# Optimization experiments

Measured on AMD Instinct MI355X. Metric: run time of the kernel, lower is better.

Reference implementation:

```python
import jax, jax.numpy as jnp
import numpy as np

B, S, D, H, F, V, K = 8, 1024, 1024, 16, 4096, 8192, 64
HD = D // H
ALPHA = 0.1


def layernorm(x, g, b, eps=1e-5):
    mu = jnp.mean(x, axis=-1, keepdims=True)
    var = jnp.var(x, axis=-1, keepdims=True)
    return (x - mu) * jax.lax.rsqrt(var + eps) * g + b


def setup_inputs() -> dict:
    key = jax.random.key(0)
    ks = jax.random.split(key, 16)
    s = lambda fan: 1.0 / np.sqrt(fan)
    inp = {
        "x": jax.random.normal(ks[0], (B, S, D), jnp.float32),
        "token_ids": jax.random.randint(ks[1], (B, S), 0, V),
        "pmi": jax.random.normal(ks[2], (V, V), jnp.float32) * 0.1,
        "Wq": jax.random.normal(ks[3], (D, D), jnp.float32) * s(D),
        "bq": jnp.zeros((D,), jnp.float32),
        "Wk": jax.random.normal(ks[4], (D, D), jnp.float32) * s(D),
        "bk": jnp.zeros((D,), jnp.float32),
        "Wv": jax.random.normal(ks[5], (D, D), jnp.float32) * s(D),
        "bv": jnp.zeros((D,), jnp.float32),
        "Wo": jax.random.normal(ks[6], (D, D), jnp.float32) * s(D),
        "bo": jnp.zeros((D,), jnp.float32),
        "W1": jax.random.normal(ks[7], (D, F), jnp.float32) * s(D),
        "b1": jnp.zeros((F,), jnp.float32),
        "W2": jax.random.normal(ks[8], (F, D), jnp.float32) * s(F),
        "b2": jnp.zeros((D,), jnp.float32),
        "g1": jnp.ones((D,), jnp.float32),
        "be1": jnp.zeros((D,), jnp.float32),
        "g2": jnp.ones((D,), jnp.float32),
        "be2": jnp.zeros((D,), jnp.float32),
    }
    return inp


def reference(x, token_ids, pmi, Wq, bq, Wk, bk, Wv, bv, Wo, bo,
              W1, b1, W2, b2, g1, be1, g2, be2):
    # --- SparseStatAttention: QK^T + alpha*PMI bias, top-k mask, softmax ---
    q = (x @ Wq + bq).reshape(B, S, H, HD)
    k = (x @ Wk + bk).reshape(B, S, H, HD)
    v = (x @ Wv + bv).reshape(B, S, H, HD)
    scores = jnp.einsum("bihd,bjhd->bhij", q, k) / np.sqrt(HD)  # [B,H,S,S]
    bias = pmi[token_ids[:, :, None], token_ids[:, None, :]]     # [B,S,S]
    scores = scores + ALPHA * bias[:, None, :, :]
    # top-k sparsification per query row (threshold at k-th largest value)
    kth = jax.lax.top_k(scores, K)[0][..., -1:]
    scores = jnp.where(scores >= kth, scores, -jnp.inf)
    w = jax.nn.softmax(scores, axis=-1)
    attn = jnp.einsum("bhij,bjhd->bihd", w, v).reshape(B, S, D)
    attn = attn @ Wo + bo
    # --- residual + norm1 (dropout is identity in eval) ---
    h = layernorm(x + attn, g1, be1)
    # --- GELU FFN (torch nn.GELU default = exact erf) ---
    ff = jax.nn.gelu(h @ W1 + b1, approximate=False) @ W2 + b2
    return layernorm(h + ff, g2, be2)
```

## Files before the change

### kernel.cpp

```cpp
#include <hip/hip_runtime.h>
#include <cstdint>
#include <cstddef>

#define B_   8
#define S_   1024
#define D_   1024
#define H_   16
#define HD_  64
#define F_   4096
#define V_   8192
#define KTOP 64

typedef unsigned short ushort_t;
typedef __attribute__((ext_vector_type(8))) short short8;
typedef __attribute__((ext_vector_type(8))) _Float16 half8;
typedef __attribute__((ext_vector_type(4))) float floatx4;
typedef __attribute__((ext_vector_type(4))) unsigned int uintx4;
typedef __attribute__((ext_vector_type(4))) float floatv4;
typedef __attribute__((ext_vector_type(4))) unsigned short ushortx4;
typedef __attribute__((ext_vector_type(8))) unsigned short ushortx8;

__device__ __forceinline__ ushort_t f2bf(float f) {
    unsigned int u = __builtin_bit_cast(unsigned int, f);
    u += 0x7fffu + ((u >> 16) & 1u);
    return (ushort_t)(u >> 16);
}
__device__ __forceinline__ float bf2f(ushort_t u) {
    unsigned int x = ((unsigned int)u) << 16;
    return __builtin_bit_cast(float, x);
}
__device__ __forceinline__ ushort_t f2h(float f) {
    _Float16 h = (_Float16)f;
    return __builtin_bit_cast(ushort_t, h);
}
__device__ __forceinline__ float h2f(ushort_t u) {
    return (float)__builtin_bit_cast(_Float16, u);
}

__device__ __forceinline__ void gload_lds16(const ushort_t* g, ushort_t* lds_base) {
    __builtin_amdgcn_global_load_lds(
        (const __attribute__((address_space(1))) unsigned int*)g,
        (__attribute__((address_space(3))) unsigned int*)lds_base,
        16, 0, 0);
}

__global__ __launch_bounds__(256) void cast_x_kernel(const float* __restrict__ x,
                                                     ushort_t* __restrict__ xb) {
    int gid = blockIdx.x * 256 + threadIdx.x;
    floatv4 v = ((const floatv4*)x)[gid];
    ushortx4 o;
    o[0] = f2bf(v[0]); o[1] = f2bf(v[1]); o[2] = f2bf(v[2]); o[3] = f2bf(v[3]);
    ((ushortx4*)xb)[gid] = o;
}

__global__ void transpose_cast_kernel(const float* __restrict__ W, ushort_t* __restrict__ WT,
                                      int K, int N, float scale) {
    __shared__ float tile[32][33];
    int n0 = blockIdx.x * 32, k0 = blockIdx.y * 32;
    #pragma unroll
    for (int i = threadIdx.y; i < 32; i += 8)
        tile[i][threadIdx.x] = W[(size_t)(k0 + i) * N + n0 + threadIdx.x];
    __syncthreads();
    #pragma unroll
    for (int i = threadIdx.y; i < 32; i += 8)
        WT[(size_t)(n0 + i) * K + k0 + threadIdx.x] = f2bf(tile[threadIdx.x][i] * scale);
}

__global__ __launch_bounds__(256) void pack_bias3_kernel(const float* __restrict__ bq,
                                                         const float* __restrict__ bk,
                                                         const float* __restrict__ bv,
                                                         float* __restrict__ o) {
    int i = blockIdx.x * 256 + threadIdx.x;
    float v = (i < 1024) ? bq[i] * 0.125f : (i < 2048) ? bk[i - 1024] : bv[i - 2048];
    o[i] = v;
}

__global__ __launch_bounds__(256) void bias_gather_kernel(const int* __restrict__ tok,
                                                          const float* __restrict__ pmi,
                                                          ushort_t* __restrict__ biasb) {
    int b = blockIdx.x >> 10;
    int i = blockIdx.x & (S_ - 1);
    int ti = tok[b * S_ + i];
    const float* prow = pmi + (size_t)ti * V_;
    #pragma unroll
    for (int it = 0; it < 4; it++) {
        int j = threadIdx.x + it * 256;
        int tj = tok[b * S_ + j];
        biasb[(size_t)blockIdx.x * S_ + j] = f2h(0.1f * prow[tj]);
    }
}

__global__ __launch_bounds__(256) void transpose_v_kernel(const ushort_t* __restrict__ v,
                                                          ushort_t* __restrict__ vT) {
    __shared__ ushort_t t[64 * 72];
    int bh = blockIdx.x >> 4;
    int s0 = (blockIdx.x & 15) * 64;
    #pragma unroll
    for (int it = 0; it < 2; it++) {
        int idx = threadIdx.x + it * 256;
        int sl = idx >> 3, dg = (idx & 7) * 8;
        *(uintx4*)&t[sl * 72 + dg] = *(const uintx4*)&v[((size_t)bh * S_ + s0 + sl) * HD_ + dg];
    }
    __syncthreads();
    #pragma unroll
    for (int it = 0; it < 2; it++) {
        int idx = threadIdx.x + it * 256;
        int dl = idx >> 3, sg = (idx & 7) * 8;
        ushortx8 o;
        #pragma unroll
        for (int i = 0; i < 8; i++) o[i] = f2h(bf2f(t[(sg + i) * 72 + dl]));
        *(ushortx8*)&vT[((size_t)bh * HD_ + dl) * S_ + s0 + sg] = o;
    }
}

__global__ __launch_bounds__(256) void gemm_bt(const ushort_t* __restrict__ A,
                                               const ushort_t* __restrict__ BT,
                                               const float* __restrict__ bias,
                                               ushort_t* __restrict__ C,
                                               int M, int N, int K, int ep) {
    __shared__ ushort_t As[2][128 * 32];
    __shared__ ushort_t Bs[2][128 * 32];

    const int tid = threadIdx.x;
    const int wid = tid >> 6, lane = tid & 63;
    const int quad = lane >> 4, r = lane & 15;
    const int wr = wid >> 1, wc = wid & 1;
    const int m0 = blockIdx.y * 128, n0 = blockIdx.x * 128;

    floatx4 acc[4][4];
    #pragma unroll
    for (int a = 0; a < 4; a++)
        #pragma unroll
        for (int b = 0; b < 4; b++) acc[a][b] = (floatx4){0.f, 0.f, 0.f, 0.f};

    const int srow = wid * 16 + (lane >> 2);
    const int scol = (lane & 3) * 8;
    const ushort_t* Ag0 = A + (size_t)(m0 + srow) * K + scol;
    const ushort_t* Ag1 = A + (size_t)(m0 + 64 + srow) * K + scol;
    const ushort_t* Bg0 = BT + (size_t)(n0 + srow) * K + scol;
    const ushort_t* Bg1 = BT + (size_t)(n0 + 64 + srow) * K + scol;
    const int d0 = (wid * 16) * 32;
    const int d1 = (64 + wid * 16) * 32;

    gload_lds16(Ag0, &As[0][d0]);
    gload_lds16(Ag1, &As[0][d1]);
    gload_lds16(Bg0, &Bs[0][d0]);
    gload_lds16(Bg1, &Bs[0][d1]);
    __syncthreads();

    int cur = 0;
    for (int k0 = 0; k0 < K; k0 += 32) {
        const int nxt = cur ^ 1;
        if (k0 + 32 < K) {
            gload_lds16(Ag0 + k0 + 32, &As[nxt][d0]);
            gload_lds16(Ag1 + k0 + 32, &As[nxt][d1]);
            gload_lds16(Bg0 + k0 + 32, &Bs[nxt][d0]);
            gload_lds16(Bg1 + k0 + 32, &Bs[nxt][d1]);
        }
        short8 af[4], bf[4];
        #pragma unroll
        for (int t = 0; t < 4; t++)
            af[t] = *(const short8*)&As[cur][(wr * 64 + t * 16 + r) * 32 + quad * 8];
        #pragma unroll
        for (int t = 0; t < 4; t++)
            bf[t] = *(const short8*)&Bs[cur][(wc * 64 + t * 16 + r) * 32 + quad * 8];
        #pragma unroll
        for (int tm = 0; tm < 4; tm++)
            #pragma unroll
            for (int tn = 0; tn < 4; tn++)
                acc[tm][tn] = __builtin_amdgcn_mfma_f32_16x16x32_bf16(af[tm], bf[tn], acc[tm][tn], 0, 0, 0);
        __syncthreads();
        cur = nxt;
    }

    #pragma unroll
    for (int tm = 0; tm < 4; tm++) {
        #pragma unroll
        for (int tn = 0; tn < 4; tn++) {
            const int n = n0 + wc * 64 + tn * 16 + r;
            const float bv = bias[n];
            #pragma unroll
            for (int i2 = 0; i2 < 4; i2++) {
                const int m = m0 + wr * 64 + tm * 16 + quad * 4 + i2;
                float v = acc[tm][tn][i2] + bv;
                if (ep == 1) v = 0.5f * v * (1.0f + erff(v * 0.70710678118654752f));
                size_t idx;
                if (ep == 2) {
                    int tensor = n >> 10, nn = n & 1023;
                    idx = (size_t)tensor * (B_ * S_ * D_)
                        + (((size_t)(m >> 10) * H_ + (nn >> 6)) * S_ + (m & (S_ - 1))) * HD_ + (nn & (HD_ - 1));
                } else {
                    idx = (size_t)m * N + n;
                }
                C[idx] = f2bf(v);
            }
        }
    }
}

__global__ __launch_bounds__(256) void attn_kernel(const ushort_t* __restrict__ q,
                                                   const ushort_t* __restrict__ k,
                                                   const ushort_t* __restrict__ vT,
                                                   const ushort_t* __restrict__ biasb,
                                                   ushort_t* __restrict__ attnb) {
    extern __shared__ char smem[];
    ushort_t* Sm = (ushort_t*)smem;
    _Float16* Smh = (_Float16*)smem;

    const int bid = blockIdx.x;
    const int b = bid >> 10;
    const int h = (bid >> 6) & (H_ - 1);
    const int i0 = (bid & 63) * 16;
    const int tid = threadIdx.x;
    const int wid = tid >> 6, lane = tid & 63;
    const int quad = lane >> 4, r = lane & 15;

    const size_t bh = (size_t)b * H_ + h;
    const ushort_t* qbase = q + bh * S_ * HD_;
    const ushort_t* kbase = k + bh * S_ * HD_;
    const ushort_t* vbase = vT + bh * HD_ * S_;
    const ushort_t* bsrc = biasb + ((size_t)b * S_ + i0) * S_;

    #pragma unroll
    for (int c8 = 0; c8 < 8; c8++) {
        int c = wid * 8 + c8;
        int row = c >> 1, half = c & 1;
        int xr = row & 7;
        gload_lds16(bsrc + (size_t)row * S_ + half * 512 + (lane ^ xr) * 8,
                    Sm + row * 1024 + half * 512);
    }
    short8 aq0 = *(const short8*)&qbase[(size_t)(i0 + r) * HD_ + quad * 8];
    short8 aq1 = *(const short8*)&qbase[(size_t)(i0 + r) * HD_ + 32 + quad * 8];
    __syncthreads();

    const int low3 = 2 * wid + (quad >> 1);
    const int labase = r * 1024 + ((low3 ^ (r & 7)) << 3) + (quad & 1) * 4;
    const ushort_t* kpl = kbase + (size_t)(wid * 16 + r) * HD_ + quad * 8;
    #pragma unroll 4
    for (int t = 0; t < 16; t++) {
        const int la = labase + t * 64;
        ushortx4 bi = *(const ushortx4*)&Sm[la];
        floatx4 acc;
        acc[0] = h2f(bi[0]); acc[1] = h2f(bi[1]); acc[2] = h2f(bi[2]); acc[3] = h2f(bi[3]);
        const ushort_t* kp = kpl + (size_t)t * 64 * HD_;
        short8 b0 = *(const short8*)kp;
        short8 b1 = *(const short8*)(kp + 32);
        acc = __builtin_amdgcn_mfma_f32_16x16x32_bf16(b0, aq0, acc, 0, 0, 0);
        acc = __builtin_amdgcn_mfma_f32_16x16x32_bf16(b1, aq1, acc, 0, 0, 0);
        ushortx4 so;
        so[0] = f2h(acc[0]); so[1] = f2h(acc[1]); so[2] = f2h(acc[2]); so[3] = f2h(acc[3]);
        *(ushortx4*)&Sm[la] = so;
    }
    __syncthreads();

    for (int rr = 0; rr < 4; rr++) {
        int row = wid * 4 + rr;
        ushort_t* Srow = Sm + row * 1024;
        ushortx8 u0 = *(const ushortx8*)&Srow[lane * 8];
        ushortx8 u1 = *(const ushortx8*)&Srow[(64 + lane) * 8];
        unsigned int kk[16];
        unsigned int lmax = 0u;
        #pragma unroll
        for (int t = 0; t < 8; t++) {
            unsigned int ua = u0[t];
            kk[t] = ua ^ ((ua & 0x8000u) ? 0xFFFFu : 0x8000u);
            lmax = kk[t] > lmax ? kk[t] : lmax;
            unsigned int ub = u1[t];
            kk[8 + t] = ub ^ ((ub & 0x8000u) ? 0xFFFFu : 0x8000u);
            lmax = kk[8 + t] > lmax ? kk[8 + t] : lmax;
        }
        unsigned int M = lmax, T0 = lmax;
        #pragma unroll
        for (int off = 32; off; off >>= 1) {
            unsigned int om = (unsigned int)__shfl_xor((int)M, off);
            unsigned int ot = (unsigned int)__shfl_xor((int)T0, off);
            M = om > M ? om : M;
            T0 = ot < T0 ? ot : T0;
        }
        float mx = h2f((ushort_t)((M & 0x8000u) ? (M ^ 0x8000u) : (~M & 0xFFFFu)));
        unsigned int T;
        int hb;
        unsigned int diff = T0 ^ M;
        if (diff == 0u) { T = M; hb = -1; }
        else { hb = 31 - __builtin_clz(diff); T = M & ~((2u << hb) - 1u); }
        for (int bit = hb; bit >= 0; bit--) {
            unsigned int trial = T | (1u << bit);
            int c = 0;
            #pragma unroll
            for (int t = 0; t < 16; t++)
                c += __popcll(__ballot(kk[t] >= trial));
            if (c >= KTOP) {
                T = trial;
                if (c == KTOP) break;
            }
        }
        float ev[16]; float sum = 0.f;
        #pragma unroll
        for (int t = 0; t < 8; t++) {
            float sa = h2f((ushort_t)u0[t]);
            float ea = (kk[t] >= T) ? __expf(sa - mx) : 0.f;
            ev[t] = ea; sum += ea;
            float sb = h2f((ushort_t)u1[t]);
            float eb = (kk[8 + t] >= T) ? __expf(sb - mx) : 0.f;
            ev[8 + t] = eb; sum += eb;
        }
        #pragma unroll
        for (int off = 32; off; off >>= 1) sum += __shfl_xor(sum, off);
        float inv = 1.f / sum;
        ushortx8 w0, w1;
        #pragma unroll
        for (int t = 0; t < 8; t++) {
            w0[t] = f2h(ev[t] * inv);
            w1[t] = f2h(ev[8 + t] * inv);
        }
        *(ushortx8*)&Srow[lane * 8] = w0;
        *(ushortx8*)&Srow[(64 + lane) * 8] = w1;
    }
    __syncthreads();

    floatx4 o0 = (floatx4){0.f, 0.f, 0.f, 0.f};
    floatx4 o1 = (floatx4){0.f, 0.f, 0.f, 0.f};
    const _Float16* Srowp = Smh + (size_t)r * 1024;
    const int xr = r & 7;
    const ushort_t* vrow = vbase + (size_t)(wid * 16 + r) * S_;
    #pragma unroll 4
    for (int ks2 = 0; ks2 < 16; ks2++) {
        int ks = ks2 * 2;
        half8 wa0 = *(const half8*)&Srowp[((ks * 4 + quad) ^ xr) << 3];
        half8 wa1 = *(const half8*)&Srowp[(((ks + 1) * 4 + quad) ^ xr) << 3];
        half8 vb0 = *(const half8*)&vrow[ks * 32 + quad * 8];
        half8 vb1 = *(const half8*)&vrow[(ks + 1) * 32 + quad * 8];
        o0 = __builtin_amdgcn_mfma_f32_16x16x32_f16(wa0, vb0, o0, 0, 0, 0);
        o1 = __builtin_amdgcn_mfma_f32_16x16x32_f16(wa1, vb1, o1, 0, 0, 0);
    }
    floatx4 oacc = o0 + o1;
    #pragma unroll
    for (int i2 = 0; i2 < 4; i2++) {
        int row = quad * 4 + i2;
        attnb[((size_t)b * S_ + i0 + row) * D_ + h * HD_ + wid * 16 + r] = f2bf(oacc[i2]);
    }
}

__global__ __launch_bounds__(256) void ln1_kernel(const float* __restrict__ x,
                                                  const ushort_t* __restrict__ t,
                                                  const float* __restrict__ g,
                                                  const float* __restrict__ be,
                                                  ushort_t* __restrict__ hb) {
    int row = blockIdx.x, tid = threadIdx.x;
    const float* xr = x + (size_t)row * D_;
    const ushort_t* tr = t + (size_t)row * D_;
    float v[4]; float s = 0.f, s2 = 0.f;
    #pragma unroll
    for (int it = 0; it < 4; it++) {
        int j = tid + it * 256;
        v[it] = xr[j] + bf2f(tr[j]);
        s += v[it]; s2 += v[it] * v[it];
    }
    #pragma unroll
    for (int off = 32; off; off >>= 1) { s += __shfl_xor(s, off); s2 += __shfl_xor(s2, off); }
    __shared__ float rs[4], rq[4];
    if ((tid & 63) == 0) { rs[tid >> 6] = s; rq[tid >> 6] = s2; }
    __syncthreads();
    s = rs[0] + rs[1] + rs[2] + rs[3];
    s2 = rq[0] + rq[1] + rq[2] + rq[3];
    float mu = s * (1.f / D_);
    float var = s2 * (1.f / D_) - mu * mu;
    float rstd = rsqrtf(var + 1e-5f);
    #pragma unroll
    for (int it = 0; it < 4; it++) {
        int j = tid + it * 256;
        hb[(size_t)row * D_ + j] = f2bf((v[it] - mu) * rstd * g[j] + be[j]);
    }
}

__global__ __launch_bounds__(256) void ln2_kernel(const ushort_t* __restrict__ hbuf,
                                                  const ushort_t* __restrict__ t,
                                                  const float* __restrict__ g,
                                                  const float* __restrict__ be,
                                                  float* __restrict__ out) {
    int row = blockIdx.x, tid = threadIdx.x;
    const ushort_t* hr = hbuf + (size_t)row * D_;
    const ushort_t* tr = t + (size_t)row * D_;
    float v[4]; float s = 0.f, s2 = 0.f;
    #pragma unroll
    for (int it = 0; it < 4; it++) {
        int j = tid + it * 256;
        v[it] = bf2f(hr[j]) + bf2f(tr[j]);
        s += v[it]; s2 += v[it] * v[it];
    }
    #pragma unroll
    for (int off = 32; off; off >>= 1) { s += __shfl_xor(s, off); s2 += __shfl_xor(s2, off); }
    __shared__ float rs[4], rq[4];
    if ((tid & 63) == 0) { rs[tid >> 6] = s; rq[tid >> 6] = s2; }
    __syncthreads();
    s = rs[0] + rs[1] + rs[2] + rs[3];
    s2 = rq[0] + rq[1] + rq[2] + rq[3];
    float mu = s * (1.f / D_);
    float var = s2 * (1.f / D_) - mu * mu;
    float rstd = rsqrtf(var + 1e-5f);
    #pragma unroll
    for (int it = 0; it < 4; it++) {
        int j = tid + it * 256;
        out[(size_t)row * D_ + j] = (v[it] - mu) * rstd * g[j] + be[j];
    }
}

extern "C" void kernel_launch(void* const* d_in, const int* in_sizes, int n_in,
                              void* d_out, int out_size, void* d_ws, size_t ws_size,
                              hipStream_t stream) {
    (void)in_sizes; (void)n_in; (void)out_size; (void)ws_size;
    const float* x   = (const float*)d_in[0];
    const int*   tok = (const int*)d_in[1];
    const float* pmi = (const float*)d_in[2];
    const float* Wq  = (const float*)d_in[3];
    const float* bq  = (const float*)d_in[4];
    const float* Wk  = (const float*)d_in[5];
    const float* bk  = (const float*)d_in[6];
    const float* Wv  = (const float*)d_in[7];
    const float* bv  = (const float*)d_in[8];
    const float* Wo  = (const float*)d_in[9];
    const float* bo  = (const float*)d_in[10];
    const float* W1  = (const float*)d_in[11];
    const float* b1  = (const float*)d_in[12];
    const float* W2  = (const float*)d_in[13];
    const float* b2  = (const float*)d_in[14];
    const float* g1  = (const float*)d_in[15];
    const float* be1 = (const float*)d_in[16];
    const float* g2  = (const float*)d_in[17];
    const float* be2 = (const float*)d_in[18];
    float* out = (float*)d_out;

    char* ws = (char*)d_ws;
    size_t off = 0;
    auto alloc = [&](size_t bytes) { char* p = ws + off; off += (bytes + 255) & ~(size_t)255; return p; };
    const size_t BSD = (size_t)B_ * S_ * D_;
    ushort_t* xb     = (ushort_t*)alloc(BSD * 2);
    ushort_t* WqkvT  = (ushort_t*)alloc((size_t)3 * D_ * D_ * 2);
    ushort_t* WoT    = (ushort_t*)alloc((size_t)D_ * D_ * 2);
    ushort_t* W1T    = (ushort_t*)alloc((size_t)D_ * F_ * 2);
    ushort_t* W2T    = (ushort_t*)alloc((size_t)F_ * D_ * 2);
    float*    bqkv   = (float*)alloc(3072 * 4);
    ushort_t* qkvb   = (ushort_t*)alloc(3 * BSD * 2);
    ushort_t* vT     = (ushort_t*)alloc(BSD * 2);
    ushort_t* biasb  = (ushort_t*)alloc((size_t)B_ * S_ * S_ * 2);
    ushort_t* extra  = (ushort_t*)alloc(BSD * 2);
    (void)extra;
    ushort_t* qb    = qkvb;
    ushort_t* kb    = qkvb + BSD;
    ushort_t* vb    = qkvb + 2 * BSD;
    ushort_t* attnb = xb;
    ushort_t* tbuf  = qb;
    ushort_t* hb    = kb;
    ushort_t* ffb   = vb;

    const size_t attn_lds = 16 * 1024 * 2;

    cast_x_kernel<<<8192, 256, 0, stream>>>(x, xb);
    transpose_cast_kernel<<<dim3(32, 32), dim3(32, 8), 0, stream>>>(Wq, WqkvT, D_, D_, 0.125f);
    transpose_cast_kernel<<<dim3(32, 32), dim3(32, 8), 0, stream>>>(Wk, WqkvT + (size_t)D_ * D_, D_, D_, 1.0f);
    transpose_cast_kernel<<<dim3(32, 32), dim3(32, 8), 0, stream>>>(Wv, WqkvT + (size_t)2 * D_ * D_, D_, D_, 1.0f);
    transpose_cast_kernel<<<dim3(32, 32), dim3(32, 8), 0, stream>>>(Wo, WoT, D_, D_, 1.0f);
    transpose_cast_kernel<<<dim3(128, 32), dim3(32, 8), 0, stream>>>(W1, W1T, D_, F_, 1.0f);
    transpose_cast_kernel<<<dim3(32, 128), dim3(32, 8), 0, stream>>>(W2, W2T, F_, D_, 1.0f);
    pack_bias3_kernel<<<12, 256, 0, stream>>>(bq, bk, bv, bqkv);
    bias_gather_kernel<<<B_ * S_, 256, 0, stream>>>(tok, pmi, biasb);

    gemm_bt<<<dim3(24, 64), 256, 0, stream>>>(xb, WqkvT, bqkv, qkvb, B_ * S_, 3 * D_, D_, 2);
    transpose_v_kernel<<<B_ * H_ * (S_ / 64), 256, 0, stream>>>(vb, vT);

    attn_kernel<<<B_ * H_ * (S_ / 16), 256, attn_lds, stream>>>(qb, kb, vT, biasb, attnb);

    gemm_bt<<<dim3(8, 64), 256, 0, stream>>>(attnb, WoT, bo, tbuf, B_ * S_, D_, D_, 0);
    ln1_kernel<<<B_ * S_, 256, 0, stream>>>(x, tbuf, g1, be1, hb);
    gemm_bt<<<dim3(32, 64), 256, 0, stream>>>(hb, W1T, b1, ffb, B_ * S_, F_, D_, 1);
    gemm_bt<<<dim3(8, 64), 256, 0, stream>>>(ffb, W2T, b2, tbuf, B_ * S_, D_, F_, 0);
    ln2_kernel<<<B_ * S_, 256, 0, stream>>>(hb, tbuf, g2, be2, out);
}
```

Measured before the change: 1.100 ms.

## Double attention block to 512 threads with split-K PV reduction

Raises the attention kernel from 4 to 8 waves per 16-row query block. Each phase is redistributed: bias load, QK^T tiles, the top-k/softmax rows, and the PV product, which is now split along the key dimension across two wave groups. Partial outputs are combined through shared memory. The aim is more latency hiding per block, at the cost of extra barriers, a shared-memory reduction, and possibly fewer resident blocks per CU.

```diff
diff --git a/kernel.cpp b/kernel.cpp
--- a/kernel.cpp
+++ b/kernel.cpp
@@ -198,7 +198,7 @@
     }
 }
 
-__global__ __launch_bounds__(256) void attn_kernel(const ushort_t* __restrict__ q,
+__global__ __launch_bounds__(512) void attn_kernel(const ushort_t* __restrict__ q,
                                                    const ushort_t* __restrict__ k,
                                                    const ushort_t* __restrict__ vT,
                                                    const ushort_t* __restrict__ biasb,
@@ -222,8 +222,8 @@
     const ushort_t* bsrc = biasb + ((size_t)b * S_ + i0) * S_;
 
     #pragma unroll
-    for (int c8 = 0; c8 < 8; c8++) {
-        int c = wid * 8 + c8;
+    for (int c8 = 0; c8 < 4; c8++) {
+        int c = wid * 4 + c8;
         int row = c >> 1, half = c & 1;
         int xr = row & 7;
         gload_lds16(bsrc + (size_t)row * S_ + half * 512 + (lane ^ xr) * 8,
@@ -233,16 +233,18 @@
     short8 aq1 = *(const short8*)&qbase[(size_t)(i0 + r) * HD_ + 32 + quad * 8];
     __syncthreads();
 
-    const int low3 = 2 * wid + (quad >> 1);
-    const int labase = r * 1024 + ((low3 ^ (r & 7)) << 3) + (quad & 1) * 4;
+    const int q1 = quad >> 1;
+    const int xr0 = r & 7;
+    const int labase = r * 1024 + ((((wid & 3) * 2 + q1) ^ xr0) << 3)
+                     + ((wid >> 2) << 6) + (quad & 1) * 4;
     const ushort_t* kpl = kbase + (size_t)(wid * 16 + r) * HD_ + quad * 8;
-    #pragma unroll 4
-    for (int t = 0; t < 16; t++) {
-        const int la = labase + t * 64;
+    #pragma unroll
+    for (int t = 0; t < 8; t++) {
+        const int la = labase + t * 128;
         ushortx4 bi = *(const ushortx4*)&Sm[la];
         floatx4 acc;
         acc[0] = h2f(bi[0]); acc[1] = h2f(bi[1]); acc[2] = h2f(bi[2]); acc[3] = h2f(bi[3]);
-        const ushort_t* kp = kpl + (size_t)t * 64 * HD_;
+        const ushort_t* kp = kpl + (size_t)t * 128 * HD_;
         short8 b0 = *(const short8*)kp;
         short8 b1 = *(const short8*)(kp + 32);
         acc = __builtin_amdgcn_mfma_f32_16x16x32_bf16(b0, aq0, acc, 0, 0, 0);
@@ -253,8 +255,8 @@
     }
     __syncthreads();
 
-    for (int rr = 0; rr < 4; rr++) {
-        int row = wid * 4 + rr;
+    for (int rr = 0; rr < 2; rr++) {
+        int row = wid * 2 + rr;
         ushort_t* Srow = Sm + row * 1024;
         ushortx8 u0 = *(const ushortx8*)&Srow[lane * 8];
         ushortx8 u1 = *(const ushortx8*)&Srow[(64 + lane) * 8];
@@ -318,14 +320,15 @@
     }
     __syncthreads();
 
+    const int dt = wid & 3, ksh = wid >> 2;
     floatx4 o0 = (floatx4){0.f, 0.f, 0.f, 0.f};
     floatx4 o1 = (floatx4){0.f, 0.f, 0.f, 0.f};
     const _Float16* Srowp = Smh + (size_t)r * 1024;
     const int xr = r & 7;
-    const ushort_t* vrow = vbase + (size_t)(wid * 16 + r) * S_;
-    #pragma unroll 4
-    for (int ks2 = 0; ks2 < 16; ks2++) {
-        int ks = ks2 * 2;
+    const ushort_t* vrow = vbase + (size_t)(dt * 16 + r) * S_;
+    #pragma unroll
+    for (int kss = 0; kss < 8; kss++) {
+        int ks = ksh * 16 + kss * 2;
         half8 wa0 = *(const half8*)&Srowp[((ks * 4 + quad) ^ xr) << 3];
         half8 wa1 = *(const half8*)&Srowp[(((ks + 1) * 4 + quad) ^ xr) << 3];
         half8 vb0 = *(const half8*)&vrow[ks * 32 + quad * 8];
@@ -334,10 +337,21 @@
         o1 = __builtin_amdgcn_mfma_f32_16x16x32_f16(wa1, vb1, o1, 0, 0, 0);
     }
     floatx4 oacc = o0 + o1;
-    #pragma unroll
-    for (int i2 = 0; i2 < 4; i2++) {
-        int row = quad * 4 + i2;
-        attnb[((size_t)b * S_ + i0 + row) * D_ + h * HD_ + wid * 16 + r] = f2bf(oacc[i2]);
+    __syncthreads();
+    float* red = (float*)smem;
+    if (ksh == 1) {
+        #pragma unroll
+        for (int i2 = 0; i2 < 4; i2++)
+            red[dt * 256 + (quad * 4 + i2) * 16 + r] = oacc[i2];
+    }
+    __syncthreads();
+    if (ksh == 0) {
+        #pragma unroll
+        for (int i2 = 0; i2 < 4; i2++) {
+            int row = quad * 4 + i2;
+            float v = oacc[i2] + red[dt * 256 + row * 16 + r];
+            attnb[((size_t)b * S_ + i0 + row) * D_ + h * HD_ + dt * 16 + r] = f2bf(v);
+        }
     }
 }
 
@@ -468,7 +482,7 @@
     gemm_bt<<<dim3(24, 64), 256, 0, stream>>>(xb, WqkvT, bqkv, qkvb, B_ * S_, 3 * D_, D_, 2);
     transpose_v_kernel<<<B_ * H_ * (S_ / 64), 256, 0, stream>>>(vb, vT);
 
-    attn_kernel<<<B_ * H_ * (S_ / 16), 256, attn_lds, stream>>>(qb, kb, vT, biasb, attnb);
+    attn_kernel<<<B_ * H_ * (S_ / 16), 512, attn_lds, stream>>>(qb, kb, vT, biasb, attnb);
 
     gemm_bt<<<dim3(8, 64), 256, 0, stream>>>(attnb, WoT, bo, tbuf, B_ * S_, D_, D_, 0);
     ln1_kernel<<<B_ * S_, 256, 0, stream>>>(x, tbuf, g1, be1, hb);
```

Measured after the change: 1.081 ms. No clear change (-1.7%).
